# Optimization experiments

Hardware: AMD Instinct MI355X
Metric: run time of the kernel (lower is better)

## Reference

```python
import jax, jax.numpy as jnp
import numpy as np
import math

B, T, C = 2, 2048, 1024
H = 16            # n_head
RATIO = 4         # ratio_kv
HKV = H // RATIO  # n_head_kv = 4
HD = C // H       # head_dim = 64
G = H // HKV      # query heads per kv head = 4


def _alibi_slopes(n_heads):
    # n_heads must be a power of 2 here (H=16)
    assert math.log2(n_heads).is_integer()
    start = 2.0 ** (-(2.0 ** (-(math.log2(n_heads) - 3))))
    return np.array([start * (start ** i) for i in range(n_heads)], dtype=np.float32)


def setup_inputs() -> dict:
    key = jax.random.key(0)
    ks = jax.random.split(key, 5)
    return {
        "x": jax.random.normal(ks[0], (B, T, C), dtype=jnp.float32),
        "Wq": jax.random.normal(ks[1], (C, C), dtype=jnp.float32) * 0.02,
        "Wk": jax.random.normal(ks[2], (C, HKV * HD), dtype=jnp.float32) * 0.02,
        "Wv": jax.random.normal(ks[3], (C, HKV * HD), dtype=jnp.float32) * 0.02,
        "Wo": jax.random.normal(ks[4], (C, C), dtype=jnp.float32) * 0.02,
    }


def reference(x, Wq, Wk, Wv, Wo):
    # GQA causal attention with ALiBi bias (flash-disabled fallback path).
    # q: [B,HKV,G,T,HD] (grouped query heads), k/v: [B,HKV,T,HD]
    q = (x @ Wq).reshape(B, T, H, HD).transpose(0, 2, 1, 3).reshape(B, HKV, G, T, HD)
    k = (x @ Wk).reshape(B, T, HKV, HD).transpose(0, 2, 1, 3)
    v = (x @ Wv).reshape(B, T, HKV, HD).transpose(0, 2, 1, 3)

    scale = 1.0 / math.sqrt(HD)
    att = jnp.einsum('bkgtd,bksd->bkgts', q, k) * scale  # [B,HKV,G,T,T]

    # ALiBi: original repeats alibi(n_head) by G and truncates to n_head,
    # so query head h uses slope get_slopes(H)[h // G] == slopes[:HKV] per kv group.
    slopes = jnp.asarray(_alibi_slopes(H))[:HKV]          # [HKV]
    pos = jnp.arange(T)
    rel = (pos[None, :] - pos[:, None]).astype(jnp.float32)  # [T,T], rel[i,j]=j-i
    bias = slopes[:, None, None] * rel                    # [HKV,T,T]
    causal = jnp.triu(jnp.full((T, T), -jnp.inf, dtype=jnp.float32), 1)

    att = att + bias[None, :, None] + causal
    att = jax.nn.softmax(att.astype(jnp.float32), axis=-1).astype(q.dtype)

    y = jnp.einsum('bkgts,bksd->bkgtd', att, v)           # [B,HKV,G,T,HD]
    y = y.reshape(B, H, T, HD).transpose(0, 2, 1, 3).reshape(B, T, C)
    return y @ Wo
```

## Files before the change

### kernel.cpp

```cpp
#include <hip/hip_runtime.h>
#include <hip/hip_bf16.h>
#include <math.h>

#define B_ 2
#define T_ 2048
#define C_ 1024
#define H_ 16
#define HKV_ 4
#define G_ 4
#define HD_ 64
#define KVC_ 256
#define NQKV_ 1536
#define NQT_ 32

typedef __attribute__((ext_vector_type(8))) short bf16x8;
typedef __attribute__((ext_vector_type(4))) float f32x4;

static __device__ inline short f2bf(float f) {
    __hip_bfloat16 h = __float2bfloat16(f);
    short s;
    __builtin_memcpy(&s, &h, 2);
    return s;
}
static __device__ inline short f2bf_trunc(float f) {
    unsigned int u;
    __builtin_memcpy(&u, &f, 4);
    return (short)(u >> 16);
}
static __device__ inline float bf2f(short s) {
    unsigned int u = ((unsigned int)(unsigned short)s) << 16;
    float f;
    __builtin_memcpy(&f, &u, 4);
    return f;
}

static __device__ inline void gload_lds16(const short* g, short* lds) {
    __builtin_amdgcn_global_load_lds(
        (const __attribute__((address_space(1))) unsigned int*)g,
        (__attribute__((address_space(3))) unsigned int*)lds, 16, 0, 0);
}

__global__ __launch_bounds__(256) void cast_bf16(
    const float* __restrict__ in, short* __restrict__ out, int n)
{
    const int i = (blockIdx.x * 256 + threadIdx.x) * 8;
    if (i >= n) return;
    const float4 a = *(const float4*)(in + i);
    const float4 b = *(const float4*)(in + i + 4);
    bf16x8 o;
    o[0] = f2bf(a.x); o[1] = f2bf(a.y); o[2] = f2bf(a.z); o[3] = f2bf(a.w);
    o[4] = f2bf(b.x); o[5] = f2bf(b.y); o[6] = f2bf(b.z); o[7] = f2bf(b.w);
    *(bf16x8*)(out + i) = o;
}

__global__ __launch_bounds__(256) void w_transpose(
    const float* __restrict__ Wq, const float* __restrict__ Wk,
    const float* __restrict__ Wv, const float* __restrict__ Wo,
    short* __restrict__ Wt, short* __restrict__ Wot)
{
    const int z = blockIdx.z;
    const float* in;
    short* out;
    int N;
    if (z == 0)      { in = Wq; out = Wt;                     N = C_; }
    else if (z == 1) { in = Wk; out = Wt + C_ * C_;           N = KVC_; }
    else if (z == 2) { in = Wv; out = Wt + (C_ + KVC_) * C_;  N = KVC_; }
    else             { in = Wo; out = Wot;                    N = C_; }
    const int n0 = blockIdx.x * 32;
    if (n0 >= N) return;
    __shared__ float t[32][33];
    const int tx = threadIdx.x, ty = threadIdx.y;
    const int k0 = blockIdx.y * 32;
    #pragma unroll
    for (int j = 0; j < 4; j++)
        t[ty + j * 8][tx] = in[(size_t)(k0 + ty + j * 8) * N + n0 + tx];
    __syncthreads();
    #pragma unroll
    for (int j = 0; j < 4; j++)
        out[(size_t)(n0 + ty + j * 8) * C_ + k0 + tx] = f2bf(t[tx][ty + j * 8]);
}

template <bool OUT_BF16>
__global__ __launch_bounds__(256) void gemm_bf16(
    const short* __restrict__ A, const short* __restrict__ Bt,
    void* __restrict__ Cout, int M, int N, int K)
{
    __shared__ short As[2][128 * 32];
    __shared__ short Bs[2][128 * 32];
    const int tid = threadIdx.x;
    const int wave = tid >> 6, lane = tid & 63;
    const int l15 = lane & 15, quad = lane >> 4;
    const int row0 = blockIdx.y * 128, col0 = blockIdx.x * 128;
    const int wr = (wave >> 1) * 64, wc = (wave & 1) * 64;
    const int sr = lane >> 2, kof = (lane & 3) * 8;

    f32x4 acc[4][4];
    #pragma unroll
    for (int i = 0; i < 4; i++)
        #pragma unroll
        for (int j = 0; j < 4; j++)
            acc[i][j] = (f32x4){0.f, 0.f, 0.f, 0.f};

#define GSTAGE(KT, BUF) do {                                                   \
        _Pragma("unroll")                                                      \
        for (int i_ = 0; i_ < 2; i_++) {                                       \
            const int rr = i_ * 64 + wave * 16;                                \
            gload_lds16(A + (size_t)(row0 + rr + sr) * K + (KT) + kof,         \
                        &As[BUF][rr * 32]);                                    \
            gload_lds16(Bt + (size_t)(col0 + rr + sr) * K + (KT) + kof,        \
                        &Bs[BUF][rr * 32]);                                    \
        }                                                                      \
    } while (0)

    GSTAGE(0, 0);
    asm volatile("s_waitcnt vmcnt(0)" ::: "memory");
    __builtin_amdgcn_s_barrier();

    int cur = 0;
    const int nkt = K >> 5;
    for (int t = 0; t < nkt; ++t) {
        if (t + 1 < nkt) GSTAGE((t + 1) * 32, cur ^ 1);

        bf16x8 af[4], bfr[4];
        #pragma unroll
        for (int mt = 0; mt < 4; mt++)
            af[mt] = *(const bf16x8*)&As[cur][(wr + mt * 16 + l15) * 32 + quad * 8];
        #pragma unroll
        for (int nt = 0; nt < 4; nt++)
            bfr[nt] = *(const bf16x8*)&Bs[cur][(wc + nt * 16 + l15) * 32 + quad * 8];
        #pragma unroll
        for (int mt = 0; mt < 4; mt++)
            #pragma unroll
            for (int nt = 0; nt < 4; nt++)
                acc[mt][nt] = __builtin_amdgcn_mfma_f32_16x16x32_bf16(
                    af[mt], bfr[nt], acc[mt][nt], 0, 0, 0);

        asm volatile("s_waitcnt vmcnt(0)" ::: "memory");
        __builtin_amdgcn_s_barrier();
        cur ^= 1;
    }
#undef GSTAGE

    #pragma unroll
    for (int mt = 0; mt < 4; mt++) {
        #pragma unroll
        for (int r = 0; r < 4; r++) {
            const size_t row = row0 + wr + mt * 16 + quad * 4 + r;
            #pragma unroll
            for (int nt = 0; nt < 4; nt++) {
                const size_t col = col0 + wc + nt * 16 + l15;
                if (OUT_BF16)
                    ((short*)Cout)[row * N + col] = f2bf(acc[mt][nt][r]);
                else
                    ((float*)Cout)[row * N + col] = acc[mt][nt][r];
            }
        }
    }
}

__global__ __launch_bounds__(256) void kv_tile(
    const short* __restrict__ QKV, short* __restrict__ Kt, short* __restrict__ Vt)
{
    __shared__ short Ls[64 * 72];
    const int jt = blockIdx.x;
    const int bk = blockIdx.y;
    const int b = bk >> 2, kh = bk & 3;
    const int tid = threadIdx.x;
    const int key = tid >> 2, d16 = (tid & 3) * 16;
    const size_t src = (size_t)(b * T_ + jt * 64 + key) * NQKV_ + C_ + kh * 64 + d16;
    const size_t tbase = (size_t)(bk * 32 + jt) * 4096;

    {
        const int db0 = (tid & 3) * 2, db1 = db0 + 1;
        *(bf16x8*)(Kt + tbase + key * 64 + ((db0 ^ (key & 7)) * 8)) =
            *(const bf16x8*)(QKV + src);
        *(bf16x8*)(Kt + tbase + key * 64 + ((db1 ^ (key & 7)) * 8)) =
            *(const bf16x8*)(QKV + src + 8);
    }
    *(bf16x8*)&Ls[key * 72 + d16]     = *(const bf16x8*)(QKV + src + KVC_);
    *(bf16x8*)&Ls[key * 72 + d16 + 8] = *(const bf16x8*)(QKV + src + KVC_ + 8);
    __syncthreads();
    const int d = tid >> 2, k16 = (tid & 3) * 16;
    bf16x8 o0, o1;
    #pragma unroll
    for (int i = 0; i < 8; i++) o0[i] = Ls[(k16 + i) * 72 + d];
    #pragma unroll
    for (int i = 0; i < 8; i++) o1[i] = Ls[(k16 + 8 + i) * 72 + d];
    const int kb0 = (tid & 3) * 2, kb1 = kb0 + 1;
    *(bf16x8*)(Vt + tbase + d * 64 + ((kb0 ^ (d & 7)) * 8)) = o0;
    *(bf16x8*)(Vt + tbase + d * 64 + ((kb1 ^ (d & 7)) * 8)) = o1;
}

#define LSTR 72

__global__ __launch_bounds__(256) void attn_mfma(
    const short* __restrict__ QKV, const short* __restrict__ Ktg,
    const short* __restrict__ Vtg, short* __restrict__ Y)
{
    const int qx = blockIdx.x;
    const int bh = blockIdx.y;
    const int qtL = qx, qtH = NQT_ - 1 - qx;
    const int b = bh >> 4, h = bh & 15, kh = h >> 2;
    const float slope2 = exp2f(-0.5f * (float)(kh + 1)) * 1.44269504f;
    const int tid = threadIdx.x;
    const int wave = tid >> 6, lane = tid & 63;
    const int l15 = lane & 15, quad = lane >> 4;
    const int lswz = (l15 & 7) * 8;

    __shared__ short Ks[4096];
    __shared__ short Vs[4096];
    __shared__ short Ps[4 * 32 * LSTR];
    short* Pw = &Ps[wave * 32 * LSTR];
    const int wswz = ((quad >> 1) & 1) << 4;
    const int rswz = ((l15 >> 3) & 1) << 4;

    const size_t bT = (size_t)b * T_;
    const size_t tb0 = (size_t)((b * HKV_ + kh) * 32) * 4096;
    const int qrow0H = qtH * 64 + wave * 16;
    const int qrow0L = qtL * 64 + wave * 16;

    const float qscale = 0.125f * 1.44269504f;
    bf16x8 qfH[2], qfL[2];
    #pragma unroll
    for (int k0 = 0; k0 < 2; k0++) {
        const short* qpH = QKV + (bT + qrow0H + l15) * NQKV_ + h * 64;
        const short* qpL = QKV + (bT + qrow0L + l15) * NQKV_ + h * 64;
        bf16x8 rH = *(const bf16x8*)(qpH + k0 * 32 + quad * 8);
        bf16x8 rL = *(const bf16x8*)(qpL + k0 * 32 + quad * 8);
        #pragma unroll
        for (int j = 0; j < 8; j++) {
            qfH[k0][j] = f2bf(bf2f(rH[j]) * qscale);
            qfL[k0][j] = f2bf(bf2f(rL[j]) * qscale);
        }
    }

    const short one_s = (short)0x3F80;
    const bf16x8 ones = {one_s, one_s, one_s, one_s, one_s, one_s, one_s, one_s};

    f32x4 OaccH[4], OaccL[4], laccH, laccL;
    #pragma unroll
    for (int nt = 0; nt < 4; nt++) {
        OaccH[nt] = (f32x4){0.f, 0.f, 0.f, 0.f};
        OaccL[nt] = (f32x4){0.f, 0.f, 0.f, 0.f};
    }
    laccH = (f32x4){0.f, 0.f, 0.f, 0.f};
    laccL = (f32x4){0.f, 0.f, 0.f, 0.f};

    for (int jtk = 0; jtk <= qtH; jtk++) {
        __syncthreads();
        {
            const short* Ktile = Ktg + tb0 + (size_t)jtk * 4096;
            const short* Vtile = Vtg + tb0 + (size_t)jtk * 4096;
            #pragma unroll
            for (int i = 0; i < 2; i++) {
                const int ch = wave * 2 + i;
                gload_lds16(Ktile + ch * 512 + lane * 8, &Ks[ch * 512]);
                gload_lds16(Vtile + ch * 512 + lane * 8, &Vs[ch * 512]);
            }
        }
        __syncthreads();

        const bool doL = (jtk <= qtL);

        bf16x8 kf[8];
        #pragma unroll
        for (int nt = 0; nt < 4; nt++)
            #pragma unroll
            for (int k0 = 0; k0 < 2; k0++)
                kf[nt * 2 + k0] = *(const bf16x8*)
                    &Ks[(nt * 16 + l15) * 64 + (((k0 * 4 + quad) * 8) ^ lswz)];

        f32x4 sH[4], sL[4];
        #pragma unroll
        for (int nt = 0; nt < 4; nt++) {
            f32x4 a = {0.f, 0.f, 0.f, 0.f};
            a = __builtin_amdgcn_mfma_f32_16x16x32_bf16(qfH[0], kf[nt*2+0], a, 0, 0, 0);
            a = __builtin_amdgcn_mfma_f32_16x16x32_bf16(qfH[1], kf[nt*2+1], a, 0, 0, 0);
            sH[nt] = a;
        }
        if (doL) {
            #pragma unroll
            for (int nt = 0; nt < 4; nt++) {
                f32x4 a = {0.f, 0.f, 0.f, 0.f};
                a = __builtin_amdgcn_mfma_f32_16x16x32_bf16(qfL[0], kf[nt*2+0], a, 0, 0, 0);
                a = __builtin_amdgcn_mfma_f32_16x16x32_bf16(qfL[1], kf[nt*2+1], a, 0, 0, 0);
                sL[nt] = a;
            }
        }

        {
            const float base = slope2 * (float)(jtk * 64 + l15 - quad * 4 - qrow0H);
            if (jtk == qtH) {
                #pragma unroll
                for (int nt = 0; nt < 4; nt++) {
                    const int colsw = ((nt * 16 + l15) ^ wswz);
                    #pragma unroll
                    for (int r = 0; r < 4; r++) {
                        const float relv = (float)(jtk * 64 + l15 - quad * 4 - qrow0H)
                                         + (float)(nt * 16 - r);
                        float p = __builtin_amdgcn_exp2f(
                            fmaf(slope2, (float)(nt * 16 - r), base) + sH[nt][r]);
                        if (relv > 0.f) p = 0.f;
                        Pw[(quad * 4 + r) * LSTR + colsw] = f2bf_trunc(p);
                    }
                }
            } else {
                #pragma unroll
                for (int nt = 0; nt < 4; nt++) {
                    const int colsw = ((nt * 16 + l15) ^ wswz);
                    #pragma unroll
                    for (int r = 0; r < 4; r++) {
                        float p = __builtin_amdgcn_exp2f(
                            fmaf(slope2, (float)(nt * 16 - r), base) + sH[nt][r]);
                        Pw[(quad * 4 + r) * LSTR + colsw] = f2bf_trunc(p);
                    }
                }
            }
        }
        if (doL) {
            const float base = slope2 * (float)(jtk * 64 + l15 - quad * 4 - qrow0L);
            if (jtk == qtL) {
                #pragma unroll
                for (int nt = 0; nt < 4; nt++) {
                    const int colsw = ((nt * 16 + l15) ^ wswz);
                    #pragma unroll
                    for (int r = 0; r < 4; r++) {
                        const float relv = (float)(jtk * 64 + l15 - quad * 4 - qrow0L)
                                         + (float)(nt * 16 - r);
                        float p = __builtin_amdgcn_exp2f(
                            fmaf(slope2, (float)(nt * 16 - r), base) + sL[nt][r]);
                        if (relv > 0.f) p = 0.f;
                        Pw[(16 + quad * 4 + r) * LSTR + colsw] = f2bf_trunc(p);
                    }
                }
            } else {
                #pragma unroll
                for (int nt = 0; nt < 4; nt++) {
                    const int colsw = ((nt * 16 + l15) ^ wswz);
                    #pragma unroll
                    for (int r = 0; r < 4; r++) {
                        float p = __builtin_amdgcn_exp2f(
                            fmaf(slope2, (float)(nt * 16 - r), base) + sL[nt][r]);
                        Pw[(16 + quad * 4 + r) * LSTR + colsw] = f2bf_trunc(p);
                    }
                }
            }
        }
        __asm__ volatile("s_waitcnt lgkmcnt(0)" ::: "memory");

        bf16x8 vf[8];
        #pragma unroll
        for (int nt = 0; nt < 4; nt++)
            #pragma unroll
            for (int k0 = 0; k0 < 2; k0++)
                vf[nt * 2 + k0] = *(const bf16x8*)
                    &Vs[(nt * 16 + l15) * 64 + (((k0 * 4 + quad) * 8) ^ lswz)];

        {
            bf16x8 pf0 = *(const bf16x8*)&Pw[l15 * LSTR + ((quad * 8) ^ rswz)];
            bf16x8 pf1 = *(const bf16x8*)&Pw[l15 * LSTR + ((32 + quad * 8) ^ rswz)];
            laccH = __builtin_amdgcn_mfma_f32_16x16x32_bf16(pf0, ones, laccH, 0, 0, 0);
            laccH = __builtin_amdgcn_mfma_f32_16x16x32_bf16(pf1, ones, laccH, 0, 0, 0);
            #pragma unroll
            for (int nt = 0; nt < 4; nt++) {
                OaccH[nt] = __builtin_amdgcn_mfma_f32_16x16x32_bf16(
                    pf0, vf[nt*2+0], OaccH[nt], 0, 0, 0);
                OaccH[nt] = __builtin_amdgcn_mfma_f32_16x16x32_bf16(
                    pf1, vf[nt*2+1], OaccH[nt], 0, 0, 0);
            }
        }
        if (doL) {
            bf16x8 pf0 = *(const bf16x8*)&Pw[(16 + l15) * LSTR + ((quad * 8) ^ rswz)];
            bf16x8 pf1 = *(const bf16x8*)&Pw[(16 + l15) * LSTR + ((32 + quad * 8) ^ rswz)];
            laccL = __builtin_amdgcn_mfma_f32_16x16x32_bf16(pf0, ones, laccL, 0, 0, 0);
            laccL = __builtin_amdgcn_mfma_f32_16x16x32_bf16(pf1, ones, laccL, 0, 0, 0);
            #pragma unroll
            for (int nt = 0; nt < 4; nt++) {
                OaccL[nt] = __builtin_amdgcn_mfma_f32_16x16x32_bf16(
                    pf0, vf[nt*2+0], OaccL[nt], 0, 0, 0);
                OaccL[nt] = __builtin_amdgcn_mfma_f32_16x16x32_bf16(
                    pf1, vf[nt*2+1], OaccL[nt], 0, 0, 0);
            }
        }
    }

    #pragma unroll
    for (int r = 0; r < 4; r++) {
        const float invH = 1.f / laccH[r];
        const float invL = 1.f / laccL[r];
        const int rowH = qrow0H + quad * 4 + r;
        const int rowL = qrow0L + quad * 4 + r;
        short* ypH = Y + (bT + rowH) * C_ + h * 64 + l15;
        short* ypL = Y + (bT + rowL) * C_ + h * 64 + l15;
        #pragma unroll
        for (int nt = 0; nt < 4; nt++) {
            ypH[nt * 16] = f2bf(OaccH[nt][r] * invH);
            ypL[nt * 16] = f2bf(OaccL[nt][r] * invL);
        }
    }
}

extern "C" void kernel_launch(void* const* d_in, const int* in_sizes, int n_in,
                              void* d_out, int out_size, void* d_ws, size_t ws_size,
                              hipStream_t stream) {
    const float* x  = (const float*)d_in[0];
    const float* Wq = (const float*)d_in[1];
    const float* Wk = (const float*)d_in[2];
    const float* Wv = (const float*)d_in[3];
    const float* Wo = (const float*)d_in[4];
    float* out = (float*)d_out;

    const int M = B_ * T_;
    short* xb  = (short*)d_ws;
    short* Wt  = xb  + (size_t)M * C_;
    short* Wot = Wt  + (size_t)NQKV_ * C_;
    short* QKV = Wot + (size_t)C_ * C_;
    short* Yb  = QKV + (size_t)M * NQKV_;
    short* Ktg = Yb  + (size_t)M * C_;
    short* Vtg = Ktg + (size_t)8 * 32 * 4096;

    cast_bf16<<<dim3(M * C_ / (256 * 8)), dim3(256), 0, stream>>>(x, xb, M * C_);
    w_transpose<<<dim3(32, 32, 4), dim3(32, 8), 0, stream>>>(Wq, Wk, Wv, Wo, Wt, Wot);

    gemm_bf16<true><<<dim3(NQKV_ / 128, M / 128), dim3(256), 0, stream>>>(
        xb, Wt, QKV, M, NQKV_, C_);
    kv_tile<<<dim3(32, 8), dim3(256), 0, stream>>>(QKV, Ktg, Vtg);
    attn_mfma<<<dim3(NQT_ / 2, B_ * H_), dim3(256), 0, stream>>>(QKV, Ktg, Vtg, Yb);
    gemm_bf16<false><<<dim3(C_ / 128, M / 128), dim3(256), 0, stream>>>(
        Yb, Wot, out, M, C_, C_);
}
```

Measured before the change: 178.1 us.

## Load K/V fragments directly from global in MFMA layout with register prefetch

The kv_tile kernel now writes K and V tiles in a fragment-major layout that matches the MFMA operand order, so each lane reads its bf16x8 fragment with one contiguous global load. The attention kernel drops the shared-memory K/V staging and both __syncthreads per tile. It prefetches the next tile's K and V fragments into registers after their current use, overlapping global latency with the softmax and PV work. This uses more registers and relies on cache hits for the per-wave redundant global reads, since all four waves load the same fragments.

```diff
diff --git a/kernel.cpp b/kernel.cpp
--- a/kernel.cpp
+++ b/kernel.cpp
@@ -171,11 +171,11 @@
     const size_t tbase = (size_t)(bk * 32 + jt) * 4096;
 
     {
-        const int db0 = (tid & 3) * 2, db1 = db0 + 1;
-        *(bf16x8*)(Kt + tbase + key * 64 + ((db0 ^ (key & 7)) * 8)) =
-            *(const bf16x8*)(QKV + src);
-        *(bf16x8*)(Kt + tbase + key * 64 + ((db1 ^ (key & 7)) * 8)) =
-            *(const bf16x8*)(QKV + src + 8);
+        const int i = (key >> 4) * 2 + (d16 >> 5);
+        const int qd = (d16 & 31) >> 3;
+        short* dst = Kt + tbase + i * 512 + (qd * 16 + (key & 15)) * 8;
+        *(bf16x8*)dst         = *(const bf16x8*)(QKV + src);
+        *(bf16x8*)(dst + 128) = *(const bf16x8*)(QKV + src + 8);
     }
     *(bf16x8*)&Ls[key * 72 + d16]     = *(const bf16x8*)(QKV + src + KVC_);
     *(bf16x8*)&Ls[key * 72 + d16 + 8] = *(const bf16x8*)(QKV + src + KVC_ + 8);
@@ -186,9 +186,13 @@
     for (int i = 0; i < 8; i++) o0[i] = Ls[(k16 + i) * 72 + d];
     #pragma unroll
     for (int i = 0; i < 8; i++) o1[i] = Ls[(k16 + 8 + i) * 72 + d];
-    const int kb0 = (tid & 3) * 2, kb1 = kb0 + 1;
-    *(bf16x8*)(Vt + tbase + d * 64 + ((kb0 ^ (d & 7)) * 8)) = o0;
-    *(bf16x8*)(Vt + tbase + d * 64 + ((kb1 ^ (d & 7)) * 8)) = o1;
+    {
+        const int i = (d >> 4) * 2 + (k16 >> 5);
+        const int qk = (k16 & 31) >> 3;
+        short* dst = Vt + tbase + i * 512 + (qk * 16 + (d & 15)) * 8;
+        *(bf16x8*)dst         = o0;
+        *(bf16x8*)(dst + 128) = o1;
+    }
 }
 
 #define LSTR 72
@@ -205,10 +209,7 @@
     const int tid = threadIdx.x;
     const int wave = tid >> 6, lane = tid & 63;
     const int l15 = lane & 15, quad = lane >> 4;
-    const int lswz = (l15 & 7) * 8;
-
-    __shared__ short Ks[4096];
-    __shared__ short Vs[4096];
+
     __shared__ short Ps[4 * 32 * LSTR];
     short* Pw = &Ps[wave * 32 * LSTR];
     const int wswz = ((quad >> 1) & 1) << 4;
@@ -216,6 +217,8 @@
 
     const size_t bT = (size_t)b * T_;
     const size_t tb0 = (size_t)((b * HKV_ + kh) * 32) * 4096;
+    const short* Kt = Ktg + tb0;
+    const short* Vt = Vtg + tb0;
     const int qrow0H = qtH * 64 + wave * 16;
     const int qrow0L = qtL * 64 + wave * 16;
 
@@ -246,29 +249,17 @@
     laccH = (f32x4){0.f, 0.f, 0.f, 0.f};
     laccL = (f32x4){0.f, 0.f, 0.f, 0.f};
 
+    bf16x8 kf[8], vf[8];
+    #pragma unroll
+    for (int i = 0; i < 8; i++)
+        kf[i] = *(const bf16x8*)(Kt + i * 512 + lane * 8);
+    #pragma unroll
+    for (int i = 0; i < 8; i++)
+        vf[i] = *(const bf16x8*)(Vt + i * 512 + lane * 8);
+
     for (int jtk = 0; jtk <= qtH; jtk++) {
-        __syncthreads();
-        {
-            const short* Ktile = Ktg + tb0 + (size_t)jtk * 4096;
-            const short* Vtile = Vtg + tb0 + (size_t)jtk * 4096;
-            #pragma unroll
-            for (int i = 0; i < 2; i++) {
-                const int ch = wave * 2 + i;
-                gload_lds16(Ktile + ch * 512 + lane * 8, &Ks[ch * 512]);
-                gload_lds16(Vtile + ch * 512 + lane * 8, &Vs[ch * 512]);
-            }
-        }
-        __syncthreads();
-
         const bool doL = (jtk <= qtL);
-
-        bf16x8 kf[8];
-        #pragma unroll
-        for (int nt = 0; nt < 4; nt++)
-            #pragma unroll
-            for (int k0 = 0; k0 < 2; k0++)
-                kf[nt * 2 + k0] = *(const bf16x8*)
-                    &Ks[(nt * 16 + l15) * 64 + (((k0 * 4 + quad) * 8) ^ lswz)];
+        const int pjt = (jtk < qtH) ? jtk + 1 : qtH;
 
         f32x4 sH[4], sL[4];
         #pragma unroll
@@ -287,6 +278,10 @@
                 sL[nt] = a;
             }
         }
+
+        #pragma unroll
+        for (int i = 0; i < 8; i++)
+            kf[i] = *(const bf16x8*)(Kt + (size_t)pjt * 4096 + i * 512 + lane * 8);
 
         {
             const float base = slope2 * (float)(jtk * 64 + l15 - quad * 4 - qrow0H);
@@ -348,14 +343,6 @@
         }
         __asm__ volatile("s_waitcnt lgkmcnt(0)" ::: "memory");
 
-        bf16x8 vf[8];
-        #pragma unroll
-        for (int nt = 0; nt < 4; nt++)
-            #pragma unroll
-            for (int k0 = 0; k0 < 2; k0++)
-                vf[nt * 2 + k0] = *(const bf16x8*)
-                    &Vs[(nt * 16 + l15) * 64 + (((k0 * 4 + quad) * 8) ^ lswz)];
-
         {
             bf16x8 pf0 = *(const bf16x8*)&Pw[l15 * LSTR + ((quad * 8) ^ rswz)];
             bf16x8 pf1 = *(const bf16x8*)&Pw[l15 * LSTR + ((32 + quad * 8) ^ rswz)];
@@ -382,6 +369,10 @@
                     pf1, vf[nt*2+1], OaccL[nt], 0, 0, 0);
             }
         }
+
+        #pragma unroll
+        for (int i = 0; i < 8; i++)
+            vf[i] = *(const bf16x8*)(Vt + (size_t)pjt * 4096 + i * 512 + lane * 8);
     }
 
     #pragma unroll
```

Result: faster. 172.2 us (-3.3%).
